# Kernel tuning notes

Measured on AMD Instinct MI355X. Metric: run time of the kernel, lower is better.

The kernel has to match this reference:

```python
import jax, jax.numpy as jnp
import numpy as np

M, N, F = 512, 128, 512  # molecules, atoms per molecule, feature dim
HID, OUT = F // 4, 1


def setup_inputs() -> dict:
    key = jax.random.key(0)
    k1, k2, k3 = jax.random.split(key, 3)
    h = jax.random.normal(k1, (M, N, F), dtype=jnp.float32)
    W1 = jax.random.normal(k2, (F, HID), dtype=jnp.float32) * (1.0 / np.sqrt(F))
    b1 = jnp.zeros((HID,), dtype=jnp.float32)
    W2 = jax.random.normal(k3, (HID, OUT), dtype=jnp.float32) * (1.0 / np.sqrt(HID))
    b2 = jnp.zeros((OUT,), dtype=jnp.float32)
    return {"h": h, "W1": W1, "b1": b1, "W2": W2, "b2": b2}


def reference(h, W1, b1, W2, b2):
    # method == 'weighted_summation'
    # gate MLP: Linear -> ReLU -> Linear -> Sigmoid, per atom
    w = jax.nn.sigmoid(jax.nn.relu(h @ W1 + b1) @ W2 + b2)  # [M, N, OUT]
    # per-molecule weighted sum over atoms: mm(w_h.T, h) for each molecule,
    # concatenated along dim 0 -> [M*OUT, F] (OUT=1 -> [M, F])
    out = jnp.einsum('mno,mnf->mof', w, h)  # [M, OUT, F]
    return out.reshape(M * OUT, F)
```

## Files before the change

kernel.cpp:

```cpp
#include <hip/hip_runtime.h>
#include <hip/hip_bf16.h>


typedef unsigned short u16;
typedef unsigned int u32;
typedef __bf16 bf16x8 __attribute__((ext_vector_type(8)));
typedef float f32x4 __attribute__((ext_vector_type(4)));
typedef float f32x2 __attribute__((ext_vector_type(2)));
typedef u32 u32x4 __attribute__((ext_vector_type(4)));

#define M_MOL 512
#define N_ATOM 128
#define F_DIM 512
#define HID_DIM 128
#define ABLK 64
#define NBLK (M_MOL * 2)

static __device__ __forceinline__ u16 f2bf(float x) {
  u32 u = __float_as_uint(x);
  u32 r = (u + 0x7fffu + ((u >> 16) & 1u)) >> 16;
  return (u16)r;
}
static __device__ __forceinline__ bf16x8 pack8(u32x4 a, u32x4 b) {
  u32x4 r;
  r[0] = (a[0] >> 16) | (a[1] & 0xffff0000u);
  r[1] = (a[2] >> 16) | (a[3] & 0xffff0000u);
  r[2] = (b[0] >> 16) | (b[1] & 0xffff0000u);
  r[3] = (b[2] >> 16) | (b[3] & 0xffff0000u);
  return __builtin_bit_cast(bf16x8, r);
}

__global__ __launch_bounds__(256) void transpose_w1(const float* __restrict__ W1,
                                                    u16* __restrict__ W1Tt) {
  __shared__ float tile[64][65];
  const int k0 = blockIdx.x * 64;
  const int n0 = blockIdx.y * 64;
  const int t = threadIdx.x;
  #pragma unroll
  for (int i = 0; i < 16; ++i) {
    const int lin = i * 256 + t;
    const int lr = lin >> 6, lc = lin & 63;
    tile[lc][lr] = W1[(size_t)(k0 + lr) * HID_DIM + (n0 + lc)];
  }
  __syncthreads();
  #pragma unroll
  for (int i = 0; i < 16; ++i) {
    const int lin = i * 256 + t;
    const int wr = lin >> 6, wc = lin & 63;
    const int k = k0 + wc;
    W1Tt[(size_t)(k >> 5) * (HID_DIM * 32) + (size_t)(n0 + wr) * 32 + (k & 31)] =
        f2bf(tile[wr][wc]);
  }
}

__global__ __launch_bounds__(256, 2) void pool_partial(
    const float* __restrict__ h, const u16* __restrict__ W1Tt,
    const float* __restrict__ b1, const float* __restrict__ W2,
    const float* __restrict__ b2, float* __restrict__ part) {
  __shared__ u16 As[ABLK * F_DIM];
  __shared__ union U {
    u16 bt[2][HID_DIM * 32];
    struct {
      float w_s[ABLK];
      float _pad[2048 - ABLK];
      float red[4][F_DIM];
    } s;
  } sm;

  const int blk = blockIdx.x;
  const int tid = threadIdx.x;
  const int wv = tid >> 6;
  const int lane = tid & 63;
  const int quad = lane >> 4;
  const int cl = lane & 15;

  {
    const u32x4* hg = (const u32x4*)(h + (size_t)blk * ABLK * F_DIM);
    #pragma unroll
    for (int i = 0; i < 16; ++i) {
      const int u = i * 256 + tid;
      const int row = u >> 6;
      const int c = u & 63;
      u32x4 lo = hg[2 * u];
      u32x4 hi = hg[2 * u + 1];
      const int phys = (c & ~7) | ((c ^ row) & 7);
      *(bf16x8*)(As + row * F_DIM + phys * 8) = pack8(lo, hi);
    }
  }

  const u16* wg = W1Tt + tid * 16;
  const int brow = tid >> 1;
  const int bc0 = 2 * (tid & 1);
  u16* bw0 = sm.bt[0] + brow * 32;
  u16* bw1 = sm.bt[1] + brow * 32;
  const int bphysA = (bc0 ^ (brow & 3)) * 8;
  const int bphysB = ((bc0 + 1) ^ (brow & 3)) * 8;
  {
    u32x4 v0 = *(const u32x4*)wg;
    u32x4 v1 = *(const u32x4*)(wg + 8);
    *(u32x4*)(bw0 + bphysA) = v0;
    *(u32x4*)(bw0 + bphysB) = v1;
  }
  __syncthreads();

  f32x4 acc[8];
  #pragma unroll
  for (int t = 0; t < 8; ++t) acc[t] = (f32x4){0.f, 0.f, 0.f, 0.f};

  const int ar = wv * 16 + cl;
  const u16* aBase = As + ar * F_DIM;
  const int bq = (quad ^ (cl & 3)) * 8;

  for (int ks = 0; ks < 16; ++ks) {
    u32x4 v0, v1;
    if (ks < 15) {
      v0 = *(const u32x4*)(wg + (ks + 1) * (HID_DIM * 32));
      v1 = *(const u32x4*)(wg + (ks + 1) * (HID_DIM * 32) + 8);
    }
    const int c = ks * 4 + quad;
    const int aphys = (c & ~7) | ((c ^ ar) & 7);
    bf16x8 afr = *(const bf16x8*)(aBase + aphys * 8);
    const u16* btb = sm.bt[ks & 1];
    #pragma unroll
    for (int t = 0; t < 8; ++t) {
      bf16x8 bfr = *(const bf16x8*)(btb + (t * 16 + cl) * 32 + bq);
      acc[t] = __builtin_amdgcn_mfma_f32_16x16x32_bf16(afr, bfr, acc[t], 0, 0, 0);
    }
    if (ks < 15) {
      u16* bw = (ks & 1) ? bw0 : bw1;
      *(u32x4*)(bw + bphysA) = v0;
      *(u32x4*)(bw + bphysB) = v1;
      __syncthreads();
    }
  }

  float psum[4] = {0.f, 0.f, 0.f, 0.f};
  #pragma unroll
  for (int t = 0; t < 8; ++t) {
    const int hid = t * 16 + cl;
    const float b1v = b1[hid];
    const float w2v = W2[hid];
    #pragma unroll
    for (int r = 0; r < 4; ++r) {
      float tv = fmaxf(acc[t][r] + b1v, 0.f);
      psum[r] = fmaf(tv, w2v, psum[r]);
    }
  }
  #pragma unroll
  for (int off = 1; off < 16; off <<= 1)
    #pragma unroll
    for (int r = 0; r < 4; ++r)
      psum[r] += __shfl_xor(psum[r], off, 64);
  if (cl == 0) {
    const float b2v = b2[0];
    #pragma unroll
    for (int r = 0; r < 4; ++r)
      sm.s.w_s[wv * 16 + quad * 4 + r] = 1.f / (1.f + __expf(-(psum[r] + b2v)));
  }
  __syncthreads();

  float facc[8] = {0.f, 0.f, 0.f, 0.f, 0.f, 0.f, 0.f, 0.f};
  #pragma unroll 4
  for (int i = 0; i < 16; ++i) {
    const int row = wv * 16 + i;
    const float wn = sm.s.w_s[row];
    const int phys = (lane & ~7) | ((lane ^ row) & 7);
    bf16x8 hv = *(const bf16x8*)(As + row * F_DIM + phys * 8);
    u32x4 uv = __builtin_bit_cast(u32x4, hv);
    #pragma unroll
    for (int j = 0; j < 4; ++j) {
      facc[2 * j]     = fmaf(wn, __uint_as_float(uv[j] << 16), facc[2 * j]);
      facc[2 * j + 1] = fmaf(wn, __uint_as_float(uv[j] & 0xffff0000u), facc[2 * j + 1]);
    }
  }
  #pragma unroll
  for (int j = 0; j < 8; ++j) sm.s.red[wv][lane * 8 + j] = facc[j];
  __syncthreads();

  {
    const int f = tid * 2;
    f32x2 o;
    o[0] = sm.s.red[0][f] + sm.s.red[1][f] + sm.s.red[2][f] + sm.s.red[3][f];
    o[1] = sm.s.red[0][f + 1] + sm.s.red[1][f + 1] + sm.s.red[2][f + 1] + sm.s.red[3][f + 1];
    *(f32x2*)(part + (size_t)blk * F_DIM + f) = o;
  }
}

__global__ __launch_bounds__(256) void reduce_out(const float* __restrict__ part,
                                                  float* __restrict__ out) {
  const int m = blockIdx.x;
  const int f = threadIdx.x * 2;
  f32x2 a = *(const f32x2*)(part + (size_t)(2 * m) * F_DIM + f);
  f32x2 b = *(const f32x2*)(part + (size_t)(2 * m + 1) * F_DIM + f);
  f32x2 o;
  o[0] = a[0] + b[0];
  o[1] = a[1] + b[1];
  *(f32x2*)(out + (size_t)m * F_DIM + f) = o;
}

extern "C" void kernel_launch(void* const* d_in, const int* in_sizes, int n_in,
                              void* d_out, int out_size, void* d_ws, size_t ws_size,
                              hipStream_t stream) {
  const float* h  = (const float*)d_in[0];
  const float* W1 = (const float*)d_in[1];
  const float* b1 = (const float*)d_in[2];
  const float* W2 = (const float*)d_in[3];
  const float* b2 = (const float*)d_in[4];
  float* out = (float*)d_out;

  u16* W1Tt = (u16*)d_ws;
  float* part = (float*)((char*)d_ws + (size_t)HID_DIM * F_DIM * sizeof(u16));

  transpose_w1<<<dim3(8, 2), 256, 0, stream>>>(W1, W1Tt);
  pool_partial<<<NBLK, 256, 0, stream>>>(h, W1Tt, b1, W2, b2, part);
  reduce_out<<<M_MOL, 256, 0, stream>>>(part, out);
}
```

Before: 214.1 us.

## Halve atom tile, split hidden dim across waves, DMA W1 tiles into LDS

Atoms per block drop from 64 to 32, so there are four blocks per molecule. Wave pairs now split the hidden dimension and combine their partial gate sums through shared memory. The W1 slices are streamed straight into LDS with global_load_lds in a matching new layout, replacing register staging, and the h loads are batched ahead of the bf16 conversion. The aim is higher occupancy (3 blocks per CU) and better latency hiding, paid for with more partial results to write and reduce and an extra cross-wave reduction step.

Result: no change. 218.4 us (+2.0%).

```diff
diff --git a/kernel.cpp b/kernel.cpp
--- a/kernel.cpp
+++ b/kernel.cpp
@@ -10,11 +10,10 @@
 typedef u32 u32x4 __attribute__((ext_vector_type(4)));
 
 #define M_MOL 512
-#define N_ATOM 128
 #define F_DIM 512
 #define HID_DIM 128
-#define ABLK 64
-#define NBLK (M_MOL * 2)
+#define ABLK 32
+#define NBLK (M_MOL * 4)
 
 static __device__ __forceinline__ u16 f2bf(float x) {
   u32 u = __float_as_uint(x);
@@ -48,24 +47,20 @@
     const int lin = i * 256 + t;
     const int wr = lin >> 6, wc = lin & 63;
     const int k = k0 + wc;
-    W1Tt[(size_t)(k >> 5) * (HID_DIM * 32) + (size_t)(n0 + wr) * 32 + (k & 31)] =
+    const int hid = n0 + wr;
+    W1Tt[(size_t)(((k >> 5) * 4 + ((k >> 3) & 3)) * HID_DIM + hid) * 8 + (k & 7)] =
         f2bf(tile[wr][wc]);
   }
 }
 
-__global__ __launch_bounds__(256, 2) void pool_partial(
+__global__ __launch_bounds__(256, 3) void pool_partial(
     const float* __restrict__ h, const u16* __restrict__ W1Tt,
     const float* __restrict__ b1, const float* __restrict__ W2,
     const float* __restrict__ b2, float* __restrict__ part) {
   __shared__ u16 As[ABLK * F_DIM];
-  __shared__ union U {
-    u16 bt[2][HID_DIM * 32];
-    struct {
-      float w_s[ABLK];
-      float _pad[2048 - ABLK];
-      float red[4][F_DIM];
-    } s;
-  } sm;
+  __shared__ u16 bt[2][4096];
+  __shared__ float wred[2][ABLK];
+  __shared__ float w_s[ABLK];
 
   const int blk = blockIdx.x;
   const int tid = threadIdx.x;
@@ -73,71 +68,68 @@
   const int lane = tid & 63;
   const int quad = lane >> 4;
   const int cl = lane & 15;
+  const int strip = wv >> 1;
+  const int hh = wv & 1;
+
+  const u16* gB = W1Tt + wv * 1024 + lane * 8;
+  #define DMA_TILE(ks, buf)                                                        \
+    do {                                                                           \
+      const u16* _g = gB + (size_t)(ks) * 4096;                                    \
+      u16* _l = &bt[buf][wv * 1024];                                               \
+      __builtin_amdgcn_global_load_lds(                                            \
+          (const __attribute__((address_space(1))) u32*)(const void*)_g,           \
+          (__attribute__((address_space(3))) u32*)(void*)_l, 16, 0, 0);            \
+      __builtin_amdgcn_global_load_lds(                                            \
+          (const __attribute__((address_space(1))) u32*)(const void*)(_g + 512),   \
+          (__attribute__((address_space(3))) u32*)(void*)(_l + 512), 16, 0, 0);    \
+    } while (0)
+
+  DMA_TILE(0, 0);
 
   {
     const u32x4* hg = (const u32x4*)(h + (size_t)blk * ABLK * F_DIM);
-    #pragma unroll
-    for (int i = 0; i < 16; ++i) {
+    u32x4 L[8], H[8];
+    #pragma unroll
+    for (int i = 0; i < 8; ++i) {
       const int u = i * 256 + tid;
-      const int row = u >> 6;
-      const int c = u & 63;
-      u32x4 lo = hg[2 * u];
-      u32x4 hi = hg[2 * u + 1];
+      L[i] = hg[2 * u];
+      H[i] = hg[2 * u + 1];
+    }
+    #pragma unroll
+    for (int i = 0; i < 8; ++i) {
+      const int u = i * 256 + tid;
+      const int row = u >> 6, c = u & 63;
       const int phys = (c & ~7) | ((c ^ row) & 7);
-      *(bf16x8*)(As + row * F_DIM + phys * 8) = pack8(lo, hi);
-    }
-  }
-
-  const u16* wg = W1Tt + tid * 16;
-  const int brow = tid >> 1;
-  const int bc0 = 2 * (tid & 1);
-  u16* bw0 = sm.bt[0] + brow * 32;
-  u16* bw1 = sm.bt[1] + brow * 32;
-  const int bphysA = (bc0 ^ (brow & 3)) * 8;
-  const int bphysB = ((bc0 + 1) ^ (brow & 3)) * 8;
-  {
-    u32x4 v0 = *(const u32x4*)wg;
-    u32x4 v1 = *(const u32x4*)(wg + 8);
-    *(u32x4*)(bw0 + bphysA) = v0;
-    *(u32x4*)(bw0 + bphysB) = v1;
-  }
-  __syncthreads();
-
-  f32x4 acc[8];
-  #pragma unroll
-  for (int t = 0; t < 8; ++t) acc[t] = (f32x4){0.f, 0.f, 0.f, 0.f};
-
-  const int ar = wv * 16 + cl;
+      *(bf16x8*)(As + row * F_DIM + phys * 8) = pack8(L[i], H[i]);
+    }
+  }
+  __syncthreads();
+
+  f32x4 acc[4];
+  #pragma unroll
+  for (int t = 0; t < 4; ++t) acc[t] = (f32x4){0.f, 0.f, 0.f, 0.f};
+
+  const int ar = strip * 16 + cl;
   const u16* aBase = As + ar * F_DIM;
-  const int bq = (quad ^ (cl & 3)) * 8;
 
   for (int ks = 0; ks < 16; ++ks) {
-    u32x4 v0, v1;
-    if (ks < 15) {
-      v0 = *(const u32x4*)(wg + (ks + 1) * (HID_DIM * 32));
-      v1 = *(const u32x4*)(wg + (ks + 1) * (HID_DIM * 32) + 8);
-    }
+    if (ks < 15) DMA_TILE(ks + 1, (ks + 1) & 1);
     const int c = ks * 4 + quad;
     const int aphys = (c & ~7) | ((c ^ ar) & 7);
     bf16x8 afr = *(const bf16x8*)(aBase + aphys * 8);
-    const u16* btb = sm.bt[ks & 1];
-    #pragma unroll
-    for (int t = 0; t < 8; ++t) {
-      bf16x8 bfr = *(const bf16x8*)(btb + (t * 16 + cl) * 32 + bq);
+    const u16* bb = bt[ks & 1] + quad * (HID_DIM * 8);
+    #pragma unroll
+    for (int t = 0; t < 4; ++t) {
+      bf16x8 bfr = *(const bf16x8*)(bb + ((hh * 4 + t) * 16 + cl) * 8);
       acc[t] = __builtin_amdgcn_mfma_f32_16x16x32_bf16(afr, bfr, acc[t], 0, 0, 0);
     }
-    if (ks < 15) {
-      u16* bw = (ks & 1) ? bw0 : bw1;
-      *(u32x4*)(bw + bphysA) = v0;
-      *(u32x4*)(bw + bphysB) = v1;
-      __syncthreads();
-    }
+    if (ks < 15) __syncthreads();
   }
 
   float psum[4] = {0.f, 0.f, 0.f, 0.f};
   #pragma unroll
-  for (int t = 0; t < 8; ++t) {
-    const int hid = t * 16 + cl;
+  for (int t = 0; t < 4; ++t) {
+    const int hid = (hh * 4 + t) * 16 + cl;
     const float b1v = b1[hid];
     const float w2v = W2[hid];
     #pragma unroll
@@ -152,18 +144,20 @@
     for (int r = 0; r < 4; ++r)
       psum[r] += __shfl_xor(psum[r], off, 64);
   if (cl == 0) {
-    const float b2v = b2[0];
     #pragma unroll
     for (int r = 0; r < 4; ++r)
-      sm.s.w_s[wv * 16 + quad * 4 + r] = 1.f / (1.f + __expf(-(psum[r] + b2v)));
-  }
+      wred[hh][strip * 16 + quad * 4 + r] = psum[r];
+  }
+  __syncthreads();
+  if (tid < ABLK)
+    w_s[tid] = 1.f / (1.f + __expf(-(wred[0][tid] + wred[1][tid] + b2[0])));
   __syncthreads();
 
   float facc[8] = {0.f, 0.f, 0.f, 0.f, 0.f, 0.f, 0.f, 0.f};
-  #pragma unroll 4
-  for (int i = 0; i < 16; ++i) {
-    const int row = wv * 16 + i;
-    const float wn = sm.s.w_s[row];
+  #pragma unroll
+  for (int i = 0; i < 8; ++i) {
+    const int row = wv * 8 + i;
+    const float wn = w_s[row];
     const int phys = (lane & ~7) | ((lane ^ row) & 7);
     bf16x8 hv = *(const bf16x8*)(As + row * F_DIM + phys * 8);
     u32x4 uv = __builtin_bit_cast(u32x4, hv);
@@ -173,15 +167,16 @@
       facc[2 * j + 1] = fmaf(wn, __uint_as_float(uv[j] & 0xffff0000u), facc[2 * j + 1]);
     }
   }
-  #pragma unroll
-  for (int j = 0; j < 8; ++j) sm.s.red[wv][lane * 8 + j] = facc[j];
+  float (*red)[F_DIM] = (float (*)[F_DIM])bt;
+  #pragma unroll
+  for (int j = 0; j < 8; ++j) red[wv][lane * 8 + j] = facc[j];
   __syncthreads();
 
   {
     const int f = tid * 2;
     f32x2 o;
-    o[0] = sm.s.red[0][f] + sm.s.red[1][f] + sm.s.red[2][f] + sm.s.red[3][f];
-    o[1] = sm.s.red[0][f + 1] + sm.s.red[1][f + 1] + sm.s.red[2][f + 1] + sm.s.red[3][f + 1];
+    o[0] = red[0][f] + red[1][f] + red[2][f] + red[3][f];
+    o[1] = red[0][f + 1] + red[1][f + 1] + red[2][f + 1] + red[3][f + 1];
     *(f32x2*)(part + (size_t)blk * F_DIM + f) = o;
   }
 }
@@ -190,11 +185,13 @@
                                                   float* __restrict__ out) {
   const int m = blockIdx.x;
   const int f = threadIdx.x * 2;
-  f32x2 a = *(const f32x2*)(part + (size_t)(2 * m) * F_DIM + f);
-  f32x2 b = *(const f32x2*)(part + (size_t)(2 * m + 1) * F_DIM + f);
-  f32x2 o;
-  o[0] = a[0] + b[0];
-  o[1] = a[1] + b[1];
+  f32x2 o = (f32x2){0.f, 0.f};
+  #pragma unroll
+  for (int p = 0; p < 4; ++p) {
+    f32x2 a = *(const f32x2*)(part + (size_t)(4 * m + p) * F_DIM + f);
+    o[0] += a[0];
+    o[1] += a[1];
+  }
   *(f32x2*)(out + (size_t)m * F_DIM + f) = o;
 }
 
```
